# Optimization experiments

Hardware: AMD Instinct MI355X
Metric: run time of the kernel (lower is better)

Reference implementation:

```python
import jax, jax.numpy as jnp
import numpy as np

EMB = 1024
H = 16
HD = EMB // H  # 64
TEMP = 8.0  # sqrt(head_dim)


def setup_inputs() -> dict:
    key = jax.random.key(0)
    ks = jax.random.split(key, 7)
    B, S = 2, 2048
    s = 1.0 / np.sqrt(EMB)
    return {
        "query": jax.random.normal(ks[0], (B, S, EMB), jnp.float32),
        "key": jax.random.normal(ks[1], (B, S, EMB), jnp.float32),
        "value": jax.random.normal(ks[2], (B, S, EMB), jnp.float32),
        "Wq": jax.random.normal(ks[3], (EMB, EMB), jnp.float32) * s,
        "Wk": jax.random.normal(ks[4], (EMB, EMB), jnp.float32) * s,
        "Wv": jax.random.normal(ks[5], (EMB, EMB), jnp.float32) * s,
        "Wo": jax.random.normal(ks[6], (EMB, EMB), jnp.float32) * s,
    }


def reference(query, key, value, Wq, Wk, Wv, Wo):
    B, S, _ = query.shape
    # linear projections (torch Linear: x @ W.T), then split heads -> [B,H,S,hd]
    def proj(x, W):
        return (x @ W.T).reshape(B, -1, H, HD).transpose(0, 2, 1, 3)
    q = proj(query, Wq)
    k = proj(key, Wk)
    v = proj(value, Wv)
    # scaled dot-product attention with explicit score matrix [B,H,S,S]
    scores = jnp.einsum("bhqd,bhkd->bhqk", q, k) / TEMP
    attn = jax.nn.softmax(scores, axis=-1)
    x = jnp.einsum("bhqk,bhkd->bhqd", attn, v)
    # concat heads and final linear
    x = x.transpose(0, 2, 1, 3).reshape(B, S, H * HD)
    return x @ Wo.T
```

## Files before the change

### kernel.cpp

```cpp
#include <hip/hip_runtime.h>
#include <hip/hip_bf16.h>
#include <stdint.h>

#define SEQ   2048
#define EMB_D 1024
#define NHEAD 16
#define HDIM  64
#define MROWS 4096
#define KDIM  1024

typedef __attribute__((ext_vector_type(8)))  short          short8;
typedef __attribute__((ext_vector_type(8)))  unsigned short ushort8;
typedef __attribute__((ext_vector_type(4)))  float          f32x4;
typedef __attribute__((ext_vector_type(16))) float          f32x16;

#define LOG2E 1.4426950408889634f
#define MFIX  8.0f

__device__ __forceinline__ unsigned short f2bf(float f) {
  union { float f; uint32_t u; } v; v.f = f;
  return (unsigned short)((v.u + 0x7fffu + ((v.u >> 16) & 1u)) >> 16);
}

__device__ __forceinline__ uint32_t packbf(float a, float b) {
  union { __hip_bfloat16 h; unsigned short u; } ca, cb;
  ca.h = __float2bfloat16(a); cb.h = __float2bfloat16(b);
  return (uint32_t)ca.u | ((uint32_t)cb.u << 16);
}

__device__ __forceinline__ void gload16(const void* g, void* l) {
  __builtin_amdgcn_global_load_lds((const __attribute__((address_space(1))) void*)g,
                                   (__attribute__((address_space(3))) void*)l,
                                   16, 0, 0);
}

__device__ __forceinline__ f32x4 mfma16(short8 a, short8 b, f32x4 c) {
  return __builtin_amdgcn_mfma_f32_16x16x32_bf16(a, b, c, 0, 0, 0);
}
__device__ __forceinline__ f32x16 mfma32(short8 a, short8 b, f32x16 c) {
  return __builtin_amdgcn_mfma_f32_32x32x16_bf16(a, b, c, 0, 0, 0);
}

__device__ __forceinline__ void cvt_body(const float* __restrict__ src,
                                         unsigned short* __restrict__ dst, int i) {
  const float4* s = (const float4*)src;
  float4 a = s[2 * i], b = s[2 * i + 1];
  ushort8 o;
  o[0] = f2bf(a.x); o[1] = f2bf(a.y); o[2] = f2bf(a.z); o[3] = f2bf(a.w);
  o[4] = f2bf(b.x); o[5] = f2bf(b.y); o[6] = f2bf(b.z); o[7] = f2bf(b.w);
  *((ushort8*)dst + i) = o;
}

__global__ void cvt3_kernel(const float* __restrict__ s0, const float* __restrict__ s1,
                            const float* __restrict__ s2,
                            unsigned short* __restrict__ d0, unsigned short* __restrict__ d1,
                            unsigned short* __restrict__ d2, int n8) {
  int i = blockIdx.x * blockDim.x + threadIdx.x;
  if (i >= n8) return;
  const float* s      = blockIdx.y == 0 ? s0 : blockIdx.y == 1 ? s1 : s2;
  unsigned short* d   = blockIdx.y == 0 ? d0 : blockIdx.y == 1 ? d1 : d2;
  cvt_body(s, d, i);
}

__global__ void cvt4_kernel(const float* __restrict__ s0, const float* __restrict__ s1,
                            const float* __restrict__ s2, const float* __restrict__ s3,
                            unsigned short* __restrict__ d0, unsigned short* __restrict__ d1,
                            unsigned short* __restrict__ d2, unsigned short* __restrict__ d3,
                            int n8) {
  int i = blockIdx.x * blockDim.x + threadIdx.x;
  if (i >= n8) return;
  const float* s    = blockIdx.y == 0 ? s0 : blockIdx.y == 1 ? s1 : blockIdx.y == 2 ? s2 : s3;
  unsigned short* d = blockIdx.y == 0 ? d0 : blockIdx.y == 1 ? d1 : blockIdx.y == 2 ? d2 : d3;
  cvt_body(s, d, i);
}

__device__ __forceinline__ void gemm_tile(const unsigned short* __restrict__ A,
                                          const unsigned short* __restrict__ Bw,
                                          unsigned short* lsA, unsigned short* lsB,
                                          int m0, int n0, f32x4 acc[4][4]) {
  const int tid  = threadIdx.x;
  const int lane = tid & 63;
  const int w    = tid >> 6;
  const int wr   = w >> 1;
  const int wc   = w & 1;
  const int lr   = lane & 15;
  const int lk8  = (lane >> 4) * 8;

  for (int k0 = 0; k0 < KDIM; k0 += 32) {
#pragma unroll
    for (int c = 0; c < 2; ++c) {
      int o   = c * 4096 + w * 1024;
      int oo  = o + lane * 16;
      int row = oo >> 6;
      int ce  = (oo & 63) >> 1;
      gload16(A  + (size_t)(m0 + row) * KDIM + k0 + ce, (char*)lsA + o);
      gload16(Bw + (size_t)(n0 + row) * KDIM + k0 + ce, (char*)lsB + o);
    }
    __syncthreads();

    short8 af[4], bf_[4];
#pragma unroll
    for (int m = 0; m < 4; ++m)
      af[m] = *(const short8*)(lsA + (wr * 64 + m * 16 + lr) * 32 + lk8);
#pragma unroll
    for (int n = 0; n < 4; ++n)
      bf_[n] = *(const short8*)(lsB + (wc * 64 + n * 16 + lr) * 32 + lk8);
#pragma unroll
    for (int m = 0; m < 4; ++m)
#pragma unroll
      for (int n = 0; n < 4; ++n)
        acc[m][n] = mfma16(af[m], bf_[n], acc[m][n]);
    __syncthreads();
  }
}

__global__ __launch_bounds__(256) void gemm_qkv(const unsigned short* __restrict__ Xq,
                                                const unsigned short* __restrict__ Xk,
                                                const unsigned short* __restrict__ Xv,
                                                const unsigned short* __restrict__ Wq,
                                                const unsigned short* __restrict__ Wk,
                                                const unsigned short* __restrict__ Wv,
                                                unsigned short* __restrict__ Qb,
                                                unsigned short* __restrict__ Kb,
                                                unsigned short* __restrict__ Vt) {
  __shared__ __align__(16) unsigned short lsA[128 * 32];
  __shared__ __align__(16) unsigned short lsB[128 * 32];
  const int z = blockIdx.z;
  const unsigned short* A  = z == 0 ? Xq : z == 1 ? Xk : Xv;
  const unsigned short* Bw = z == 0 ? Wq : z == 1 ? Wk : Wv;
  const int m0 = blockIdx.y * 128;
  const int n0 = blockIdx.x * 128;

  f32x4 acc[4][4] = {};
  gemm_tile(A, Bw, lsA, lsB, m0, n0, acc);

  const int lane = threadIdx.x & 63;
  const int w    = threadIdx.x >> 6;
  const int wr = w >> 1, wc = w & 1;
  const int crow = (lane >> 4) * 4;
  const int ccol = lane & 15;
#pragma unroll
  for (int m = 0; m < 4; ++m) {
#pragma unroll
    for (int n = 0; n < 4; ++n) {
#pragma unroll
      for (int r = 0; r < 4; ++r) {
        int row = m0 + wr * 64 + m * 16 + crow + r;
        int col = n0 + wc * 64 + n * 16 + ccol;
        float vv = acc[m][n][r];
        int b = row >> 11, s = row & 2047;
        int h = col >> 6,  d = col & 63;
        if (z == 0)
          Qb[((size_t)(b * NHEAD + h) * SEQ + s) * HDIM + d] = f2bf(vv * 0.125f);
        else if (z == 1)
          Kb[((size_t)(b * NHEAD + h) * SEQ + s) * HDIM + d] = f2bf(vv);
        else
          Vt[((size_t)(b * NHEAD + h) * HDIM + d) * SEQ + s] = f2bf(vv);
      }
    }
  }
}

__global__ __launch_bounds__(256) void gemm_out(const unsigned short* __restrict__ A,
                                                const unsigned short* __restrict__ Bw,
                                                float* __restrict__ Cout) {
  __shared__ __align__(16) unsigned short lsA[128 * 32];
  __shared__ __align__(16) unsigned short lsB[128 * 32];
  const int m0 = blockIdx.y * 128;
  const int n0 = blockIdx.x * 128;
  f32x4 acc[4][4] = {};
  gemm_tile(A, Bw, lsA, lsB, m0, n0, acc);

  const int lane = threadIdx.x & 63;
  const int w    = threadIdx.x >> 6;
  const int wr = w >> 1, wc = w & 1;
  const int crow = (lane >> 4) * 4;
  const int ccol = lane & 15;
#pragma unroll
  for (int m = 0; m < 4; ++m)
#pragma unroll
    for (int n = 0; n < 4; ++n)
#pragma unroll
      for (int r = 0; r < 4; ++r) {
        int row = m0 + wr * 64 + m * 16 + crow + r;
        int col = n0 + wc * 64 + n * 16 + ccol;
        Cout[(size_t)row * EMB_D + col] = acc[m][n][r];
      }
}

__global__ __launch_bounds__(128) void attn_kernel(const unsigned short* __restrict__ Qb,
                                                   const unsigned short* __restrict__ Kb,
                                                   const unsigned short* __restrict__ Vt,
                                                   unsigned short* __restrict__ AO) {
  __shared__ float lbuf[2 * 16 * 64 + 64];
  const int lane = threadIdx.x & 63;
  const int w    = threadIdx.x >> 6;
  const int qt   = blockIdx.x & 63;
  const int bh   = blockIdx.x >> 6;
  const int b    = bh >> 4;
  const int h    = bh & 15;
  const unsigned short* Qg = Qb + (size_t)bh * SEQ * HDIM;
  const unsigned short* Kg = Kb + (size_t)bh * SEQ * HDIM;
  const unsigned short* Vg = Vt + (size_t)bh * HDIM * SEQ;

  const int ln = lane & 31;
  const int hi = lane >> 5;
  const int q0 = qt * 32;

  short8 qf[4];
#pragma unroll
  for (int ds = 0; ds < 4; ++ds)
    qf[ds] = *(const short8*)(Qg + (size_t)(q0 + ln) * HDIM + ds * 16 + hi * 8);

  f32x16 o0 = {}, o1 = {};
  float l = 0.f;

  const int kv0 = w * (SEQ / 2);
  for (int kv = kv0; kv < kv0 + SEQ / 2; kv += 32) {
    short8 kf[4];
#pragma unroll
    for (int ds = 0; ds < 4; ++ds)
      kf[ds] = *(const short8*)(Kg + (size_t)(kv + ln) * HDIM + ds * 16 + hi * 8);
    short8 vf00 = *(const short8*)(Vg + (size_t)(ln)      * SEQ + kv +      hi * 8);
    short8 vf01 = *(const short8*)(Vg + (size_t)(ln)      * SEQ + kv + 16 + hi * 8);
    short8 vf10 = *(const short8*)(Vg + (size_t)(32 + ln) * SEQ + kv +      hi * 8);
    short8 vf11 = *(const short8*)(Vg + (size_t)(32 + ln) * SEQ + kv + 16 + hi * 8);

    f32x16 st = {};
#pragma unroll
    for (int ds = 0; ds < 4; ++ds) st = mfma32(kf[ds], qf[ds], st);

    float p[16];
    float rs = 0.f;
#pragma unroll
    for (int r = 0; r < 16; ++r) { p[r] = exp2f((st[r] - MFIX) * LOG2E); rs += p[r]; }
    rs += __shfl_xor(rs, 32);
    l += rs;

    uint32_t wv_[8], sw[8];
#pragma unroll
    for (int i = 0; i < 8; ++i) wv_[i] = packbf(p[2 * i], p[2 * i + 1]);
#pragma unroll
    for (int i = 0; i < 8; ++i) sw[i] = __shfl_xor(wv_[i], 32);

    union { uint32_t u[4]; short8 s; } pb0, pb1;
    pb0.u[0] = hi ? sw[2]  : wv_[0];
    pb0.u[1] = hi ? sw[3]  : wv_[1];
    pb0.u[2] = hi ? wv_[2] : sw[0];
    pb0.u[3] = hi ? wv_[3] : sw[1];
    pb1.u[0] = hi ? sw[6]  : wv_[4];
    pb1.u[1] = hi ? sw[7]  : wv_[5];
    pb1.u[2] = hi ? wv_[6] : sw[4];
    pb1.u[3] = hi ? wv_[7] : sw[5];

    o0 = mfma32(vf00, pb0.s, o0);
    o0 = mfma32(vf01, pb1.s, o0);
    o1 = mfma32(vf10, pb0.s, o1);
    o1 = mfma32(vf11, pb1.s, o1);
  }

  if (w == 1) {
#pragma unroll
    for (int r = 0; r < 16; ++r) {
      lbuf[r * 64 + lane]        = o0[r];
      lbuf[1024 + r * 64 + lane] = o1[r];
    }
    lbuf[2048 + lane] = l;
  }
  __syncthreads();
  if (w == 0) {
    l += lbuf[2048 + lane];
    float inv = 1.0f / l;
#pragma unroll
    for (int r = 0; r < 16; ++r) {
      o0[r] += lbuf[r * 64 + lane];
      o1[r] += lbuf[1024 + r * 64 + lane];
    }
    unsigned short* orow = AO + ((size_t)b * SEQ + q0 + ln) * EMB_D + h * HDIM + hi * 4;
#pragma unroll
    for (int g = 0; g < 4; ++g) {
      uint2 d0, d1;
      d0.x = packbf(o0[4 * g + 0] * inv, o0[4 * g + 1] * inv);
      d0.y = packbf(o0[4 * g + 2] * inv, o0[4 * g + 3] * inv);
      d1.x = packbf(o1[4 * g + 0] * inv, o1[4 * g + 1] * inv);
      d1.y = packbf(o1[4 * g + 2] * inv, o1[4 * g + 3] * inv);
      *(uint2*)(orow + g * 8)      = d0;
      *(uint2*)(orow + 32 + g * 8) = d1;
    }
  }
}

extern "C" void kernel_launch(void* const* d_in, const int* in_sizes, int n_in,
                              void* d_out, int out_size, void* d_ws, size_t ws_size,
                              hipStream_t stream) {
  const float* q  = (const float*)d_in[0];
  const float* k  = (const float*)d_in[1];
  const float* v  = (const float*)d_in[2];
  const float* wq = (const float*)d_in[3];
  const float* wk = (const float*)d_in[4];
  const float* wv = (const float*)d_in[5];
  const float* wo = (const float*)d_in[6];
  float* out = (float*)d_out;

  unsigned short* p = (unsigned short*)d_ws;
  unsigned short* Xq  = p; p += (size_t)MROWS * EMB_D;
  unsigned short* Xk  = p; p += (size_t)MROWS * EMB_D;
  unsigned short* Xv  = p; p += (size_t)MROWS * EMB_D;
  unsigned short* Wqb = p; p += (size_t)EMB_D * EMB_D;
  unsigned short* Wkb = p; p += (size_t)EMB_D * EMB_D;
  unsigned short* Wvb = p; p += (size_t)EMB_D * EMB_D;
  unsigned short* Wob = p; p += (size_t)EMB_D * EMB_D;
  unsigned short* Qb  = p; p += (size_t)MROWS * EMB_D;
  unsigned short* Kb  = p; p += (size_t)MROWS * EMB_D;
  unsigned short* Vt  = p; p += (size_t)MROWS * EMB_D;
  unsigned short* AO  = p; p += (size_t)MROWS * EMB_D;

  const int nx = MROWS * EMB_D / 8;
  const int nw = EMB_D * EMB_D / 8;
  dim3 g3((nx + 255) / 256, 3);
  cvt3_kernel<<<g3, 256, 0, stream>>>(q, k, v, Xq, Xk, Xv, nx);
  dim3 g4((nw + 255) / 256, 4);
  cvt4_kernel<<<g4, 256, 0, stream>>>(wq, wk, wv, wo, Wqb, Wkb, Wvb, Wob, nw);

  dim3 gq(EMB_D / 128, MROWS / 128, 3);
  gemm_qkv<<<gq, 256, 0, stream>>>(Xq, Xk, Xv, Wqb, Wkb, Wvb, Qb, Kb, Vt);

  attn_kernel<<<2048, 128, 0, stream>>>(Qb, Kb, Vt, AO);

  dim3 gg(EMB_D / 128, MROWS / 128);
  gemm_out<<<gg, 256, 0, stream>>>(AO, Wob, out);
}
```

Measured before the change: 312.8 us.

## Restructure attention: per-wave query tiles, register double-buffered KV, XCD-aware mapping

The attention kernel now gives each of four waves its own 32-row query tile over the full KV range, which removes the split-KV reduction through LDS and the block barrier. K/V fragments are double-buffered in registers so the next tile's loads are issued before the current tile's MFMAs. Blocks are remapped so blocks sharing a head land on the same XCD, which should improve L2 reuse of K/V. The softmax scale and log2e are folded into Q at projection time, dropping the fixed-max subtraction, so exp2 is applied directly. This removes the fixed offset that guarded against overflow and adds register pressure from the second K/V buffer, which could lower occupancy.

```diff
diff --git a/kernel.cpp b/kernel.cpp
--- a/kernel.cpp
+++ b/kernel.cpp
@@ -15,7 +15,7 @@
 typedef __attribute__((ext_vector_type(16))) float          f32x16;
 
 #define LOG2E 1.4426950408889634f
-#define MFIX  8.0f
+#define QSCALE (0.125f * LOG2E)
 
 __device__ __forceinline__ unsigned short f2bf(float f) {
   union { float f; uint32_t u; } v; v.f = f;
@@ -151,7 +151,7 @@
         int b = row >> 11, s = row & 2047;
         int h = col >> 6,  d = col & 63;
         if (z == 0)
-          Qb[((size_t)(b * NHEAD + h) * SEQ + s) * HDIM + d] = f2bf(vv * 0.125f);
+          Qb[((size_t)(b * NHEAD + h) * SEQ + s) * HDIM + d] = f2bf(vv * QSCALE);
         else if (z == 1)
           Kb[((size_t)(b * NHEAD + h) * SEQ + s) * HDIM + d] = f2bf(vv);
         else
@@ -188,15 +188,69 @@
       }
 }
 
-__global__ __launch_bounds__(128) void attn_kernel(const unsigned short* __restrict__ Qb,
+__device__ __forceinline__ void load_kv(const unsigned short* __restrict__ Kg,
+                                        const unsigned short* __restrict__ Vg,
+                                        int kv, int ln, int hi,
+                                        short8 (&kf)[4], short8& v00, short8& v01,
+                                        short8& v10, short8& v11) {
+#pragma unroll
+  for (int ds = 0; ds < 4; ++ds)
+    kf[ds] = *(const short8*)(Kg + (size_t)(kv + ln) * HDIM + ds * 16 + hi * 8);
+  v00 = *(const short8*)(Vg + (size_t)(ln)      * SEQ + kv +      hi * 8);
+  v01 = *(const short8*)(Vg + (size_t)(ln)      * SEQ + kv + 16 + hi * 8);
+  v10 = *(const short8*)(Vg + (size_t)(32 + ln) * SEQ + kv +      hi * 8);
+  v11 = *(const short8*)(Vg + (size_t)(32 + ln) * SEQ + kv + 16 + hi * 8);
+}
+
+__device__ __forceinline__ void attn_tile(const short8 (&qf)[4], const short8 (&kf)[4],
+                                          const short8& vf00, const short8& vf01,
+                                          const short8& vf10, const short8& vf11,
+                                          int hi, f32x16& o0, f32x16& o1, float& l) {
+  f32x16 st = {};
+#pragma unroll
+  for (int ds = 0; ds < 4; ++ds) st = mfma32(kf[ds], qf[ds], st);
+
+  float p[16];
+  float rs = 0.f;
+#pragma unroll
+  for (int r = 0; r < 16; ++r) { p[r] = exp2f(st[r]); rs += p[r]; }
+  rs += __shfl_xor(rs, 32);
+  l += rs;
+
+  uint32_t wv_[8], sw[8];
+#pragma unroll
+  for (int i = 0; i < 8; ++i) wv_[i] = packbf(p[2 * i], p[2 * i + 1]);
+#pragma unroll
+  for (int i = 0; i < 8; ++i) sw[i] = __shfl_xor(wv_[i], 32);
+
+  union { uint32_t u[4]; short8 s; } pb0, pb1;
+  pb0.u[0] = hi ? sw[2]  : wv_[0];
+  pb0.u[1] = hi ? sw[3]  : wv_[1];
+  pb0.u[2] = hi ? wv_[2] : sw[0];
+  pb0.u[3] = hi ? wv_[3] : sw[1];
+  pb1.u[0] = hi ? sw[6]  : wv_[4];
+  pb1.u[1] = hi ? sw[7]  : wv_[5];
+  pb1.u[2] = hi ? wv_[6] : sw[4];
+  pb1.u[3] = hi ? wv_[7] : sw[5];
+
+  f32x16 t0 = o0, t1 = o1;
+  t0 = mfma32(vf00, pb0.s, t0);
+  t0 = mfma32(vf01, pb1.s, t0);
+  t1 = mfma32(vf10, pb0.s, t1);
+  t1 = mfma32(vf11, pb1.s, t1);
+  o0 = t0; o1 = t1;
+}
+
+__global__ __launch_bounds__(256) void attn_kernel(const unsigned short* __restrict__ Qb,
                                                    const unsigned short* __restrict__ Kb,
                                                    const unsigned short* __restrict__ Vt,
                                                    unsigned short* __restrict__ AO) {
-  __shared__ float lbuf[2 * 16 * 64 + 64];
   const int lane = threadIdx.x & 63;
   const int w    = threadIdx.x >> 6;
-  const int qt   = blockIdx.x & 63;
-  const int bh   = blockIdx.x >> 6;
+  const int xcd  = blockIdx.x & 7;
+  const int slot = blockIdx.x >> 3;
+  const int bh   = xcd + 8 * (slot >> 4);
+  const int qt4  = slot & 15;
   const int b    = bh >> 4;
   const int h    = bh & 15;
   const unsigned short* Qg = Qb + (size_t)bh * SEQ * HDIM;
@@ -205,7 +259,7 @@
 
   const int ln = lane & 31;
   const int hi = lane >> 5;
-  const int q0 = qt * 32;
+  const int q0 = qt4 * 128 + w * 32;
 
   short8 qf[4];
 #pragma unroll
@@ -215,78 +269,29 @@
   f32x16 o0 = {}, o1 = {};
   float l = 0.f;
 
-  const int kv0 = w * (SEQ / 2);
-  for (int kv = kv0; kv < kv0 + SEQ / 2; kv += 32) {
-    short8 kf[4];
-#pragma unroll
-    for (int ds = 0; ds < 4; ++ds)
-      kf[ds] = *(const short8*)(Kg + (size_t)(kv + ln) * HDIM + ds * 16 + hi * 8);
-    short8 vf00 = *(const short8*)(Vg + (size_t)(ln)      * SEQ + kv +      hi * 8);
-    short8 vf01 = *(const short8*)(Vg + (size_t)(ln)      * SEQ + kv + 16 + hi * 8);
-    short8 vf10 = *(const short8*)(Vg + (size_t)(32 + ln) * SEQ + kv +      hi * 8);
-    short8 vf11 = *(const short8*)(Vg + (size_t)(32 + ln) * SEQ + kv + 16 + hi * 8);
-
-    f32x16 st = {};
-#pragma unroll
-    for (int ds = 0; ds < 4; ++ds) st = mfma32(kf[ds], qf[ds], st);
-
-    float p[16];
-    float rs = 0.f;
-#pragma unroll
-    for (int r = 0; r < 16; ++r) { p[r] = exp2f((st[r] - MFIX) * LOG2E); rs += p[r]; }
-    rs += __shfl_xor(rs, 32);
-    l += rs;
-
-    uint32_t wv_[8], sw[8];
-#pragma unroll
-    for (int i = 0; i < 8; ++i) wv_[i] = packbf(p[2 * i], p[2 * i + 1]);
-#pragma unroll
-    for (int i = 0; i < 8; ++i) sw[i] = __shfl_xor(wv_[i], 32);
-
-    union { uint32_t u[4]; short8 s; } pb0, pb1;
-    pb0.u[0] = hi ? sw[2]  : wv_[0];
-    pb0.u[1] = hi ? sw[3]  : wv_[1];
-    pb0.u[2] = hi ? wv_[2] : sw[0];
-    pb0.u[3] = hi ? wv_[3] : sw[1];
-    pb1.u[0] = hi ? sw[6]  : wv_[4];
-    pb1.u[1] = hi ? sw[7]  : wv_[5];
-    pb1.u[2] = hi ? wv_[6] : sw[4];
-    pb1.u[3] = hi ? wv_[7] : sw[5];
-
-    o0 = mfma32(vf00, pb0.s, o0);
-    o0 = mfma32(vf01, pb1.s, o0);
-    o1 = mfma32(vf10, pb0.s, o1);
-    o1 = mfma32(vf11, pb1.s, o1);
+  short8 kA[4], kB[4];
+  short8 vA00, vA01, vA10, vA11, vB00, vB01, vB10, vB11;
+
+  load_kv(Kg, Vg, 0, ln, hi, kA, vA00, vA01, vA10, vA11);
+  for (int kv = 0; kv < SEQ; kv += 64) {
+    load_kv(Kg, Vg, kv + 32, ln, hi, kB, vB00, vB01, vB10, vB11);
+    attn_tile(qf, kA, vA00, vA01, vA10, vA11, hi, o0, o1, l);
+    int nkv = (kv + 64 < SEQ) ? kv + 64 : 0;
+    load_kv(Kg, Vg, nkv, ln, hi, kA, vA00, vA01, vA10, vA11);
+    attn_tile(qf, kB, vB00, vB01, vB10, vB11, hi, o0, o1, l);
   }
 
-  if (w == 1) {
-#pragma unroll
-    for (int r = 0; r < 16; ++r) {
-      lbuf[r * 64 + lane]        = o0[r];
-      lbuf[1024 + r * 64 + lane] = o1[r];
-    }
-    lbuf[2048 + lane] = l;
-  }
-  __syncthreads();
-  if (w == 0) {
-    l += lbuf[2048 + lane];
-    float inv = 1.0f / l;
-#pragma unroll
-    for (int r = 0; r < 16; ++r) {
-      o0[r] += lbuf[r * 64 + lane];
-      o1[r] += lbuf[1024 + r * 64 + lane];
-    }
-    unsigned short* orow = AO + ((size_t)b * SEQ + q0 + ln) * EMB_D + h * HDIM + hi * 4;
-#pragma unroll
-    for (int g = 0; g < 4; ++g) {
-      uint2 d0, d1;
-      d0.x = packbf(o0[4 * g + 0] * inv, o0[4 * g + 1] * inv);
-      d0.y = packbf(o0[4 * g + 2] * inv, o0[4 * g + 3] * inv);
-      d1.x = packbf(o1[4 * g + 0] * inv, o1[4 * g + 1] * inv);
-      d1.y = packbf(o1[4 * g + 2] * inv, o1[4 * g + 3] * inv);
-      *(uint2*)(orow + g * 8)      = d0;
-      *(uint2*)(orow + 32 + g * 8) = d1;
-    }
+  float inv = 1.0f / l;
+  unsigned short* orow = AO + ((size_t)b * SEQ + q0 + ln) * EMB_D + h * HDIM + hi * 4;
+#pragma unroll
+  for (int g = 0; g < 4; ++g) {
+    uint2 d0, d1;
+    d0.x = packbf(o0[4 * g + 0] * inv, o0[4 * g + 1] * inv);
+    d0.y = packbf(o0[4 * g + 2] * inv, o0[4 * g + 3] * inv);
+    d1.x = packbf(o1[4 * g + 0] * inv, o1[4 * g + 1] * inv);
+    d1.y = packbf(o1[4 * g + 2] * inv, o1[4 * g + 3] * inv);
+    *(uint2*)(orow + g * 8)      = d0;
+    *(uint2*)(orow + 32 + g * 8) = d1;
   }
 }
 
@@ -325,7 +330,7 @@
   dim3 gq(EMB_D / 128, MROWS / 128, 3);
   gemm_qkv<<<gq, 256, 0, stream>>>(Xq, Xk, Xv, Wqb, Wkb, Wvb, Qb, Kb, Vt);
 
-  attn_kernel<<<2048, 128, 0, stream>>>(Qb, Kb, Vt, AO);
+  attn_kernel<<<512, 256, 0, stream>>>(Qb, Kb, Vt, AO);
 
   dim3 gg(EMB_D / 128, MROWS / 128);
   gemm_out<<<gg, 256, 0, stream>>>(AO, Wob, out);
```

Result: faster. 296.5 us (-5.2%).
